# Kernel tuning notes

Measured on AMD Instinct MI355X. Metric: run time of the kernel, lower is better.

The kernel has to match this reference:

```python
import jax, jax.numpy as jnp
import numpy as np

B, T, F, H = 256, 256, 512, 512
DIN = 17  # 16 MLP features + 1 Y_past channel
EPS = 1e-3  # keras LayerNorm/BatchNorm default epsilon


def _glorot(key, shape):
    lim = np.sqrt(6.0 / (shape[0] + shape[-1]))
    return jax.random.uniform(key, shape, jnp.float32, -lim, lim)


def setup_inputs():
    key = jax.random.key(0)
    ks = iter(jax.random.split(key, 48))
    p = {}
    p["x"] = jax.random.normal(next(ks), (B, T, F), jnp.float32)
    p["y_past"] = jax.random.randint(next(ks), (B, T), 0, 11, jnp.int32)
    p["ln_g"] = jnp.ones((F,), jnp.float32); p["ln_b"] = jnp.zeros((F,), jnp.float32)
    for i, (a, b) in enumerate([(F, 128), (128, 64), (64, 32), (32, 16)], 1):
        p[f"w{i}"] = _glorot(next(ks), (a, b)); p[f"b{i}"] = jnp.zeros((b,), jnp.float32)
    for name, d in [("bn1", 128), ("bn2", 16)]:
        p[name + "_g"] = jnp.ones((d,), jnp.float32); p[name + "_b"] = jnp.zeros((d,), jnp.float32)
        p[name + "_m"] = jnp.zeros((d,), jnp.float32); p[name + "_v"] = jnp.ones((d,), jnp.float32)
    for pre, din in [("enc_fwd", DIN), ("enc_bwd", DIN), ("dec", H)]:
        p[pre + "_wx"] = _glorot(next(ks), (din, 4 * H))
        p[pre + "_wh"] = _glorot(next(ks), (H, 4 * H))
        p[pre + "_bias"] = jnp.zeros((4 * H,), jnp.float32)
    for pre in ["proj", "sph", "spc"]:
        p[pre + "_w"] = _glorot(next(ks), (2 * H, H)); p[pre + "_b"] = jnp.zeros((H,), jnp.float32)
    p["out_w"] = _glorot(next(ks), (H, 2)); p["out_b"] = jnp.zeros((2,), jnp.float32)
    return p


def _lstm(x_seq, wx, wh, bias):
    """Keras-order (i,f,g,o) LSTM over [B,T,Din]; returns (hs [B,T,H], hT, cT)."""
    xz = jnp.einsum('btd,dh->bth', x_seq, wx) + bias  # precompute input gates
    h0 = jnp.zeros((x_seq.shape[0], H), x_seq.dtype)
    c0 = jnp.zeros_like(h0)
    def step(carry, xz_t):
        h, c = carry
        z = xz_t + h @ wh
        i, f, g, o = jnp.split(z, 4, axis=-1)
        c = jax.nn.sigmoid(f) * c + jax.nn.sigmoid(i) * jnp.tanh(g)
        h = jax.nn.sigmoid(o) * jnp.tanh(c)
        return (h, c), h
    (hT, cT), hs = jax.lax.scan(step, (h0, c0), jnp.swapaxes(xz, 0, 1))
    return jnp.swapaxes(hs, 0, 1), hT, cT


def _forward(x, ln_g, ln_b, w1, b1, w2, b2, w3, b3, w4, b4,
             bn1_g, bn1_b, bn1_m, bn1_v, bn2_g, bn2_b, bn2_m, bn2_v,
             enc_fwd_wx, enc_fwd_wh, enc_fwd_bias,
             enc_bwd_wx, enc_bwd_wh, enc_bwd_bias,
             dec_wx, dec_wh, dec_bias,
             proj_w, proj_b, sph_w, sph_b, spc_w, spc_b, out_w, out_b, y_past):
    # LayerNorm over feature axis
    mu = jnp.mean(x, -1, keepdims=True)
    var = jnp.var(x, -1, keepdims=True)
    h = (x - mu) * jax.lax.rsqrt(var + EPS) * ln_g + ln_b
    # Dense funnel with inference-mode BatchNorm (dropout is identity)
    h = jax.nn.relu(h @ w1 + b1)
    h = (h - bn1_m) * jax.lax.rsqrt(bn1_v + EPS) * bn1_g + bn1_b
    h = jax.nn.relu(h @ w2 + b2)
    h = jax.nn.relu(h @ w3 + b3)
    h = jax.nn.relu(h @ w4 + b4)
    h = (h - bn2_m) * jax.lax.rsqrt(bn2_v + EPS) * bn2_g + bn2_b
    seq = jnp.concatenate([h, y_past.astype(jnp.float32)[..., None]], axis=-1)  # [B,T,17]
    # Bidirectional LSTM encoder
    hs_f, hf, cf = _lstm(seq, enc_fwd_wx, enc_fwd_wh, enc_fwd_bias)
    hs_b, hb, cb = _lstm(seq[:, ::-1], enc_bwd_wx, enc_bwd_wh, enc_bwd_bias)
    enc = jnp.concatenate([hs_f, hs_b[:, ::-1]], axis=-1)  # [B,T,2H]
    enc = enc @ proj_w + proj_b                             # [B,T,H]
    state_h = jnp.concatenate([hf, hb], -1) @ sph_w + sph_b
    state_c = jnp.concatenate([cf, cb], -1) @ spc_w + spc_b
    # keras Attention (dot-product, unscaled), query = state_h expanded to len 1
    scores = jnp.einsum('bh,bth->bt', state_h, enc)
    attn = jnp.einsum('bt,bth->bh', jax.nn.softmax(scores, axis=-1), enc)  # [B,H]
    # decoder LSTM runs on a length-1 sequence => single cell step
    z = attn @ dec_wx + state_h @ dec_wh + dec_bias
    i, f, g, o = jnp.split(z, 4, axis=-1)
    c = jax.nn.sigmoid(f) * state_c + jax.nn.sigmoid(i) * jnp.tanh(g)
    hdec = jax.nn.sigmoid(o) * jnp.tanh(c)
    return hdec @ out_w + out_b  # [B,2]


def reference(x, y_past, ln_g, ln_b, w1, b1, w2, b2, w3, b3, w4, b4,
              bn1_g, bn1_b, bn1_m, bn1_v, bn2_g, bn2_b, bn2_m, bn2_v,
              enc_fwd_wx, enc_fwd_wh, enc_fwd_bias,
              enc_bwd_wx, enc_bwd_wh, enc_bwd_bias,
              dec_wx, dec_wh, dec_bias,
              proj_w, proj_b, sph_w, sph_b, spc_w, spc_b, out_w, out_b):
    return _forward(x, ln_g, ln_b, w1, b1, w2, b2, w3, b3, w4, b4,
                    bn1_g, bn1_b, bn1_m, bn1_v, bn2_g, bn2_b, bn2_m, bn2_v,
                    enc_fwd_wx, enc_fwd_wh, enc_fwd_bias,
                    enc_bwd_wx, enc_bwd_wh, enc_bwd_bias,
                    dec_wx, dec_wh, dec_bias,
                    proj_w, proj_b, sph_w, sph_b, spc_w, spc_b, out_w, out_b, y_past)
```

## Files before the change

kernel.cpp:

```cpp
#include <hip/hip_runtime.h>
#include <hip/hip_bf16.h>

#define EPSK 1e-3f

using bf16x8 = __attribute__((ext_vector_type(8))) short;
using s16x4  = __attribute__((ext_vector_type(4))) short;
using f32x4  = __attribute__((ext_vector_type(4))) float;
using u32x2  = __attribute__((ext_vector_type(2))) unsigned int;

__device__ __forceinline__ float bf2f(short s) {
    union { unsigned u; float f; } x; x.u = ((unsigned)(unsigned short)s) << 16; return x.f;
}
__device__ __forceinline__ unsigned short f2bfu(float f) {
    union { float f; unsigned u; } x; x.f = f;
    unsigned r = x.u + 0x7fffu + ((x.u >> 16) & 1u);
    return (unsigned short)(r >> 16);
}
__device__ __forceinline__ float sigm(float x) { return 1.0f / (1.0f + __expf(-x)); }
__device__ __forceinline__ float ftanh(float x) {
    float e = __expf(2.0f * x);
    return 1.0f - 2.0f / (e + 1.0f);
}

__device__ __forceinline__ f32x4 load16_coh(const void* p) {
    f32x4 v;
    asm volatile("global_load_dwordx4 %0, %1, off sc0 sc1" : "=v"(v) : "v"(p) : "memory");
    return v;
}
__device__ __forceinline__ void store8_coh(void* p, u32x2 v) {
    asm volatile("global_store_dwordx2 %0, %1, off sc0 sc1" :: "v"(p), "v"(v) : "memory");
}
__device__ __forceinline__ void store8_nt(void* p, u32x2 v) {
    asm volatile("global_store_dwordx2 %0, %1, off nt" :: "v"(p), "v"(v) : "memory");
}


__global__ void cvt_f2b_kernel(__hip_bfloat16* __restrict__ dst, const float* __restrict__ src, int n)
{
    for (int i = blockIdx.x * blockDim.x + threadIdx.x; i < n; i += gridDim.x * blockDim.x)
        dst[i] = __float2bfloat16(src[i]);
}

__global__ void copy_f_kernel(float* __restrict__ dst, const float* __restrict__ src, int n)
{
    for (int i = blockIdx.x * blockDim.x + threadIdx.x; i < n; i += gridDim.x * blockDim.x)
        dst[i] = src[i];
}

#define NTJOBS 11
struct TransJobs {
    const float* src[NTJOBS];
    __hip_bfloat16* dst[NTJOBS];
    int K[NTJOBS], N[NTJOBS], kOff[NTJOBS], KD[NTJOBS];
};

__global__ __launch_bounds__(256)
void trans_tiled_kernel(TransJobs jobs)
{
    const int j = blockIdx.y;
    const int K = jobs.K[j], N = jobs.N[j];
    const int tilesN = (N + 31) >> 5;
    const int tilesK = (K + 31) >> 5;
    if ((int)blockIdx.x >= tilesN * tilesK) return;
    const int tk = blockIdx.x / tilesN, tn = blockIdx.x % tilesN;
    const int kOff = jobs.kOff[j], KD = jobs.KD[j];
    const float* src = jobs.src[j];
    __hip_bfloat16* dst = jobs.dst[j];
    __shared__ float tile[32][33];
    const int tid = threadIdx.x;
    #pragma unroll
    for (int i = 0; i < 4; ++i) {
        int e = i * 256 + tid;
        int r = e >> 5, c = e & 31;
        int k = tk * 32 + r, n = tn * 32 + c;
        tile[r][c] = (k < K && n < N) ? src[(size_t)k * N + n] : 0.f;
    }
    __syncthreads();
    #pragma unroll
    for (int i = 0; i < 4; ++i) {
        int e = i * 256 + tid;
        int rn = e >> 5, ck = e & 31;
        int n = tn * 32 + rn, k = tk * 32 + ck;
        if (k < K && n < N) dst[(size_t)n * KD + kOff + k] = __float2bfloat16(tile[ck][rn]);
    }
}


__global__ __launch_bounds__(256)
void funnel_kernel(const float* __restrict__ x, const int* __restrict__ yp,
                   const float* __restrict__ ln_g, const float* __restrict__ ln_b,
                   const __hip_bfloat16* __restrict__ w1T,
                   const float* __restrict__ b1,
                   const __hip_bfloat16* __restrict__ w2T,
                   const float* __restrict__ b2,
                   const float* __restrict__ w3, const float* __restrict__ b3,
                   const float* __restrict__ w4, const float* __restrict__ b4,
                   const float* __restrict__ bn1g, const float* __restrict__ bn1b,
                   const float* __restrict__ bn1m, const float* __restrict__ bn1v,
                   const float* __restrict__ bn2g, const float* __restrict__ bn2b,
                   const float* __restrict__ bn2m, const float* __restrict__ bn2v,
                   __hip_bfloat16* __restrict__ seqbf)
{
    __shared__ __align__(16) __hip_bfloat16 xn[16][520];
    __shared__ __align__(16) __hip_bfloat16 h1s[16][136];
    __shared__ float h2s[16][64];
    __shared__ float h3s[16][32];
    const int tid = threadIdx.x;
    const int w = tid >> 6, lane = tid & 63;
    const int l15 = lane & 15, l4 = lane >> 4;
    const int g0 = blockIdx.x * 16;

    for (int pp = 0; pp < 4; ++pp) {
        int r = pp * 4 + w;
        const float* xr = x + (size_t)(g0 + r) * 512;
        f32x4 v0 = *(const f32x4*)(xr + lane * 8);
        f32x4 v1 = *(const f32x4*)(xr + lane * 8 + 4);
        float s = v0[0]+v0[1]+v0[2]+v0[3] + v1[0]+v1[1]+v1[2]+v1[3];
        float q = v0[0]*v0[0]+v0[1]*v0[1]+v0[2]*v0[2]+v0[3]*v0[3]
                + v1[0]*v1[0]+v1[1]*v1[1]+v1[2]*v1[2]+v1[3]*v1[3];
        for (int o = 32; o; o >>= 1) { s += __shfl_xor(s, o); q += __shfl_xor(q, o); }
        float mu = s * (1.0f / 512.0f);
        float var = q * (1.0f / 512.0f) - mu * mu;
        float rs = rsqrtf(var + EPSK);
        union { unsigned short s[8]; f32x4 v; } pk;
        #pragma unroll
        for (int j = 0; j < 8; ++j) {
            int c = lane * 8 + j;
            float xv = (j < 4) ? v0[j] : v1[j - 4];
            pk.s[j] = f2bfu((xv - mu) * rs * ln_g[c] + ln_b[c]);
        }
        *(f32x4*)(&xn[r][lane * 8]) = pk.v;
    }
    __syncthreads();

    {
        f32x4 acc[2];
        acc[0] = (f32x4){0.f,0.f,0.f,0.f};
        acc[1] = (f32x4){0.f,0.f,0.f,0.f};
        #pragma unroll
        for (int kc = 0; kc < 16; ++kc) {
            bf16x8 a = *(const bf16x8*)(&xn[l15][kc * 32 + l4 * 8]);
            #pragma unroll
            for (int nf = 0; nf < 2; ++nf) {
                bf16x8 b = *(const bf16x8*)(w1T + (size_t)(w * 32 + nf * 16 + l15) * 512 + kc * 32 + l4 * 8);
                acc[nf] = __builtin_amdgcn_mfma_f32_16x16x32_bf16(a, b, acc[nf], 0, 0, 0);
            }
        }
        #pragma unroll
        for (int nf = 0; nf < 2; ++nf)
            #pragma unroll
            for (int r = 0; r < 4; ++r) {
                int row = l4 * 4 + r;
                int col = w * 32 + nf * 16 + l15;
                float v = fmaxf(acc[nf][r] + b1[col], 0.f);
                v = (v - bn1m[col]) * rsqrtf(bn1v[col] + EPSK) * bn1g[col] + bn1b[col];
                h1s[row][col] = __float2bfloat16(v);
            }
    }
    __syncthreads();

    {
        f32x4 acc = (f32x4){0.f,0.f,0.f,0.f};
        #pragma unroll
        for (int kc = 0; kc < 4; ++kc) {
            bf16x8 a = *(const bf16x8*)(&h1s[l15][kc * 32 + l4 * 8]);
            bf16x8 b = *(const bf16x8*)(w2T + (size_t)(w * 16 + l15) * 128 + kc * 32 + l4 * 8);
            acc = __builtin_amdgcn_mfma_f32_16x16x32_bf16(a, b, acc, 0, 0, 0);
        }
        #pragma unroll
        for (int r = 0; r < 4; ++r) {
            int row = l4 * 4 + r, col = w * 16 + l15;
            h2s[row][col] = fmaxf(acc[r] + b2[col], 0.f);
        }
    }
    __syncthreads();

    const int row = tid >> 4, ci = tid & 15;
    {
        float a0 = b3[ci * 2], a1 = b3[ci * 2 + 1];
        #pragma unroll 4
        for (int k = 0; k < 64; ++k) {
            float xv = h2s[row][k];
            a0 += xv * w3[k * 32 + ci * 2];
            a1 += xv * w3[k * 32 + ci * 2 + 1];
        }
        h3s[row][ci * 2] = fmaxf(a0, 0.f);
        h3s[row][ci * 2 + 1] = fmaxf(a1, 0.f);
    }
    __syncthreads();
    {
        float a = b4[ci];
        #pragma unroll
        for (int k = 0; k < 32; ++k) a += h3s[row][k] * w4[k * 16 + ci];
        float v = fmaxf(a, 0.f);
        v = (v - bn2m[ci]) * rsqrtf(bn2v[ci] + EPSK) * bn2g[ci] + bn2b[ci];
        int g = g0 + row, bb = g >> 8, tt = g & 255;
        __hip_bfloat16* sr = seqbf + ((size_t)tt * 256 + bb) * 32;
        sr[ci] = __float2bfloat16(v);
        sr[16 + ci] = (ci == 0) ? __float2bfloat16((float)yp[g]) : __float2bfloat16(0.f);
    }
}


__global__ void __launch_bounds__(256, 2)
lstm_persistent(const __hip_bfloat16* __restrict__ BTcat,
                const float* __restrict__ biasz,
                const __hip_bfloat16* __restrict__ seqbf,
                __hip_bfloat16* __restrict__ hbuf,
                float* __restrict__ cbuf,
                __hip_bfloat16* __restrict__ Aenc,
                unsigned int* __restrict__ ctrs)
{
    const int bid = blockIdx.x;
    const int g = bid & 15;
    const int dirv = g & 1;
    const int mt = g >> 1;
    const int strip = bid >> 4;
    const int tid = threadIdx.x;
    const int w = tid >> 6;
    const int lane = tid & 63;
    const int l15 = lane & 15, l4 = lane >> 4;

    __shared__ __align__(16) unsigned char Atile[32 * 1152];
    __shared__ __align__(16) float zbuf[2][4][16][36];

    float (*zb)[32][36] = (float (*)[32][36])zbuf;

    bf16x8 bw[2][17];
    {
        const __hip_bfloat16* BT = BTcat + (size_t)dirv * 2048 * 544;
        #pragma unroll
        for (int nf = 0; nf < 2; ++nf) {
            const __hip_bfloat16* bp = BT + (size_t)(w * 512 + strip * 32 + nf * 16 + l15) * 544 + l4 * 8;
            #pragma unroll
            for (int kc = 0; kc < 17; ++kc)
                bw[nf][kc] = *(const bf16x8*)(bp + kc * 32);
        }
    }

    const int rr = tid >> 3;
    const int c0 = (tid & 7) * 4;
    const int hcol0 = strip * 32 + c0;
    const int browE = mt * 32 + rr;
    const float* bias = biasz + dirv * 2048;
    const f32x4 b_i = *(const f32x4*)(bias + hcol0);
    const f32x4 b_f = *(const f32x4*)(bias + 512 + hcol0);
    const f32x4 b_g = *(const f32x4*)(bias + 1024 + hcol0);
    const f32x4 b_o = *(const f32x4*)(bias + 1536 + hcol0);

    float creg[4] = {0.f, 0.f, 0.f, 0.f};
    unsigned int* ctr = ctrs + g * 32;
    const int swzA = l15 & 7;

    for (int t = 0; t < 256; ++t) {
        const int tpos = dirv ? (255 - t) : t;

        {
            const unsigned char* hsrc = (const unsigned char*)
                (hbuf + ((size_t)(t & 1) * 2 + dirv) * 131072 + (size_t)mt * 32 * 512);
            f32x4 hv[8];
            #pragma unroll
            for (int it = 0; it < 8; ++it)
                hv[it] = load16_coh(hsrc + (it * 256 + tid) * 16);
            f32x4 sv;
            if (tid < 128) {
                const __hip_bfloat16* sp = seqbf + ((size_t)tpos * 256 + mt * 32 + (tid >> 2)) * 32 + (tid & 3) * 8;
                sv = *(const f32x4*)sp;
            }
            asm volatile("s_waitcnt vmcnt(0)" ::: "memory");
            #pragma unroll
            for (int it = 0; it < 8; ++it) {
                int c = it * 256 + tid;
                int row = c >> 6, s = c & 63;
                *(f32x4*)(Atile + row * 1152 + ((s ^ (row & 7)) << 4)) = hv[it];
            }
            if (tid < 128) {
                int row = tid >> 2, s = 64 + (tid & 3);
                *(f32x4*)(Atile + row * 1152 + ((s ^ (row & 7)) << 4)) = sv;
            }
        }
        __syncthreads();

        f32x4 acc[2][2];
        acc[0][0] = (f32x4){0.f,0.f,0.f,0.f}; acc[0][1] = (f32x4){0.f,0.f,0.f,0.f};
        acc[1][0] = (f32x4){0.f,0.f,0.f,0.f}; acc[1][1] = (f32x4){0.f,0.f,0.f,0.f};
        #pragma unroll
        for (int kc = 0; kc < 17; ++kc) {
            int swz = ((kc * 4 + l4) ^ swzA) << 4;
            bf16x8 a0 = *(const bf16x8*)(Atile + l15 * 1152 + swz);
            bf16x8 a1 = *(const bf16x8*)(Atile + (16 + l15) * 1152 + swz);
            acc[0][0] = __builtin_amdgcn_mfma_f32_16x16x32_bf16(a0, bw[0][kc], acc[0][0], 0, 0, 0);
            acc[0][1] = __builtin_amdgcn_mfma_f32_16x16x32_bf16(a0, bw[1][kc], acc[0][1], 0, 0, 0);
            acc[1][0] = __builtin_amdgcn_mfma_f32_16x16x32_bf16(a1, bw[0][kc], acc[1][0], 0, 0, 0);
            acc[1][1] = __builtin_amdgcn_mfma_f32_16x16x32_bf16(a1, bw[1][kc], acc[1][1], 0, 0, 0);
        }

        #pragma unroll
        for (int mf = 0; mf < 2; ++mf)
            #pragma unroll
            for (int nf = 0; nf < 2; ++nf)
                #pragma unroll
                for (int r = 0; r < 4; ++r)
                    zb[w][mf * 16 + l4 * 4 + r][nf * 16 + l15] = acc[mf][nf][r];
        __syncthreads();

        {
            f32x4 zi4 = *(const f32x4*)(&zb[0][rr][c0]);
            f32x4 zf4 = *(const f32x4*)(&zb[1][rr][c0]);
            f32x4 zg4 = *(const f32x4*)(&zb[2][rr][c0]);
            f32x4 zo4 = *(const f32x4*)(&zb[3][rr][c0]);
            unsigned short hb[4];
            #pragma unroll
            for (int j = 0; j < 4; ++j) {
                float iv = sigm(zi4[j] + b_i[j]);
                float fv = sigm(zf4[j] + b_f[j]);
                float gv = ftanh(zg4[j] + b_g[j]);
                float ov = sigm(zo4[j] + b_o[j]);
                float cnew = fv * creg[j] + iv * gv;
                creg[j] = cnew;
                hb[j] = f2bfu(ov * ftanh(cnew));
            }
            u32x2 hp;
            hp[0] = (unsigned)hb[0] | ((unsigned)hb[1] << 16);
            hp[1] = (unsigned)hb[2] | ((unsigned)hb[3] << 16);
            __hip_bfloat16* hdst = hbuf + ((size_t)((t + 1) & 1) * 2 + dirv) * 131072;
            store8_coh(hdst + (size_t)browE * 512 + hcol0, hp);
            store8_nt(reinterpret_cast<short*>(Aenc) + ((size_t)browE * 256 + tpos) * 1024 + dirv * 512 + hcol0, hp);
        }

        if (t < 255) {
            asm volatile("s_waitcnt vmcnt(0)" ::: "memory");
            __syncthreads();
            if (tid == 0) {
                __hip_atomic_fetch_add(ctr, 1u, __ATOMIC_RELAXED, __HIP_MEMORY_SCOPE_AGENT);
                unsigned int target = 16u * (unsigned)(t + 1);
                while (__hip_atomic_load(ctr, __ATOMIC_RELAXED, __HIP_MEMORY_SCOPE_AGENT) < target)
                    __builtin_amdgcn_s_sleep(2);
            }
            __syncthreads();
        }
    }

    *(f32x4*)(cbuf + (size_t)dirv * 131072 + (size_t)browE * 512 + hcol0) =
        (f32x4){creg[0], creg[1], creg[2], creg[3]};
}


template<int MT, int KD>
__global__ __launch_bounds__(256)
void dec_cell_kernel(const __hip_bfloat16* __restrict__ Abase,
                     const __hip_bfloat16* __restrict__ BTbase,
                     const float* __restrict__ bias,
                     const float* __restrict__ Cin,
                     float* __restrict__ HdecOut)
{
    constexpr int RB = KD * 2;
    constexpr int MF = MT / 16;
    constexpr int KSTEPS = KD / 32;
    const int strip = blockIdx.x;
    const int mt = blockIdx.y;
    const int tid = threadIdx.x;
    const int w = tid >> 6;
    const int lane = tid & 63;

    __shared__ __align__(16) unsigned char Als[MT * KD * 2];
    __shared__ float zbuf[4][MT][33];

    const __hip_bfloat16* A = Abase + (size_t)(mt * MT) * KD;
    const __hip_bfloat16* BT = BTbase;

    const unsigned char* Ac = (const unsigned char*)A;
    #pragma unroll
    for (int it = 0; it < (MT * KD * 2) / 4096; ++it) {
        int p = it * 4096 + tid * 16;
        int row = p / RB;
        int slot = (p % RB) >> 4;
        int ls = slot ^ (row & 7);
        *(f32x4*)(Als + row * RB + ls * 16) = *(const f32x4*)(Ac + p);
    }
    __syncthreads();

    f32x4 acc[MF][2];
    #pragma unroll
    for (int mf = 0; mf < MF; ++mf)
        #pragma unroll
        for (int nf = 0; nf < 2; ++nf)
            acc[mf][nf] = (f32x4){0.f,0.f,0.f,0.f};

    const int l15 = lane & 15, l4 = lane >> 4;
    #pragma unroll 4
    for (int kc = 0; kc < KSTEPS; ++kc) {
        bf16x8 a[MF], bb[2];
        int kslot = kc * 4 + l4;
        #pragma unroll
        for (int mf = 0; mf < MF; ++mf) {
            int row = mf * 16 + l15;
            a[mf] = *(const bf16x8*)(Als + row * RB + ((kslot ^ (row & 7)) << 4));
        }
        #pragma unroll
        for (int nf = 0; nf < 2; ++nf) {
            int zr = w * 512 + strip * 32 + nf * 16 + l15;
            bb[nf] = *(const bf16x8*)(BT + (size_t)zr * KD + kc * 32 + l4 * 8);
        }
        #pragma unroll
        for (int mf = 0; mf < MF; ++mf)
            #pragma unroll
            for (int nf = 0; nf < 2; ++nf)
                acc[mf][nf] = __builtin_amdgcn_mfma_f32_16x16x32_bf16(a[mf], bb[nf], acc[mf][nf], 0, 0, 0);
    }

    #pragma unroll
    for (int mf = 0; mf < MF; ++mf)
        #pragma unroll
        for (int nf = 0; nf < 2; ++nf)
            #pragma unroll
            for (int r = 0; r < 4; ++r)
                zbuf[w][mf * 16 + l4 * 4 + r][nf * 16 + l15] = acc[mf][nf][r];
    __syncthreads();

    constexpr int NE = MT * 32 / 256;
    #pragma unroll
    for (int e = 0; e < NE; ++e) {
        int idx = e * 256 + tid;
        int r = idx >> 5, col = idx & 31;
        int hcol = strip * 32 + col;
        int brow = mt * MT + r;
        float zi = zbuf[0][r][col] + bias[hcol];
        float zf = zbuf[1][r][col] + bias[512 + hcol];
        float zg = zbuf[2][r][col] + bias[1024 + hcol];
        float zo = zbuf[3][r][col] + bias[1536 + hcol];
        float iv = sigm(zi), fv = sigm(zf), gv = ftanh(zg);
        float cold = Cin[(size_t)brow * 512 + hcol];
        float cnew = fv * cold + iv * gv;
        HdecOut[(size_t)brow * 512 + hcol] = sigm(zo) * ftanh(cnew);
    }
}


__global__ __launch_bounds__(256)
void gemm_kernel(const __hip_bfloat16* __restrict__ A,
                 const __hip_bfloat16* __restrict__ BT,
                 const float* __restrict__ bias,
                 float* __restrict__ outF,
                 int M, int N, int K)
{
    const int tid = threadIdx.x;
    const int wv = tid >> 6, lane = tid & 63;
    const int wr = wv >> 1, wc = wv & 1;
    const int m0 = blockIdx.y * 64, n0 = blockIdx.x * 64;
    const int l15 = lane & 15, l4 = lane >> 4;
    f32x4 acc[2][2];
    #pragma unroll
    for (int i = 0; i < 2; ++i)
        #pragma unroll
        for (int j = 0; j < 2; ++j) acc[i][j] = (f32x4){0.f,0.f,0.f,0.f};
    for (int kc = 0; kc < K / 32; ++kc) {
        bf16x8 a[2], b[2];
        #pragma unroll
        for (int m2 = 0; m2 < 2; ++m2)
            a[m2] = *(const bf16x8*)(A + (size_t)(m0 + wr * 32 + m2 * 16 + l15) * K + kc * 32 + l4 * 8);
        #pragma unroll
        for (int n2 = 0; n2 < 2; ++n2)
            b[n2] = *(const bf16x8*)(BT + (size_t)(n0 + wc * 32 + n2 * 16 + l15) * K + kc * 32 + l4 * 8);
        #pragma unroll
        for (int m2 = 0; m2 < 2; ++m2)
            #pragma unroll
            for (int n2 = 0; n2 < 2; ++n2)
                acc[m2][n2] = __builtin_amdgcn_mfma_f32_16x16x32_bf16(a[m2], b[n2], acc[m2][n2], 0, 0, 0);
    }
    #pragma unroll
    for (int m2 = 0; m2 < 2; ++m2)
        #pragma unroll
        for (int n2 = 0; n2 < 2; ++n2)
            #pragma unroll
            for (int r = 0; r < 4; ++r) {
                int row = m0 + wr * 32 + m2 * 16 + l4 * 4 + r;
                int col = n0 + wc * 32 + n2 * 16 + l15;
                float v = acc[m2][n2][r];
                if (bias) v += bias[col];
                outF[(size_t)row * N + col] = v;
            }
}


__global__ __launch_bounds__(256)
void attn_kernel(const __hip_bfloat16* __restrict__ Aenc,
                 const float* __restrict__ qh,
                 __hip_bfloat16* __restrict__ Aactx)
{
    const int b = blockIdx.x, tid = threadIdx.x;
    __shared__ float qs[1024];
    __shared__ float sc[256];
    __shared__ float wred[4];
    for (int i = tid; i < 1024; i += 256) qs[i] = qh[(size_t)b * 1024 + i];
    __syncthreads();
    const __hip_bfloat16* ar = Aenc + ((size_t)b * 256 + tid) * 1024;
    float s = 0.f;
    for (int j8 = 0; j8 < 128; ++j8) {
        bf16x8 v = *(const bf16x8*)(ar + j8 * 8);
        #pragma unroll
        for (int e = 0; e < 8; ++e) s += bf2f(v[e]) * qs[j8 * 8 + e];
    }
    float m = s;
    for (int o = 32; o; o >>= 1) m = fmaxf(m, __shfl_xor(m, o));
    if ((tid & 63) == 0) wred[tid >> 6] = m;
    __syncthreads();
    m = fmaxf(fmaxf(wred[0], wred[1]), fmaxf(wred[2], wred[3]));
    __syncthreads();
    float ev = __expf(s - m);
    float ss = ev;
    for (int o = 32; o; o >>= 1) ss += __shfl_xor(ss, o);
    if ((tid & 63) == 0) wred[tid >> 6] = ss;
    __syncthreads();
    float tot = wred[0] + wred[1] + wred[2] + wred[3];
    sc[tid] = ev / tot;
    __syncthreads();
    float a0 = 0, a1 = 0, a2 = 0, a3 = 0;
    for (int t2 = 0; t2 < 256; ++t2) {
        float p = sc[t2];
        s16x4 v = *(const s16x4*)(Aenc + ((size_t)b * 256 + t2) * 1024 + tid * 4);
        a0 += p * bf2f(v[0]); a1 += p * bf2f(v[1]); a2 += p * bf2f(v[2]); a3 += p * bf2f(v[3]);
    }
    __hip_bfloat16* dst = Aactx + (size_t)b * 1024 + tid * 4;
    dst[0] = __float2bfloat16(a0); dst[1] = __float2bfloat16(a1);
    dst[2] = __float2bfloat16(a2); dst[3] = __float2bfloat16(a3);
}


__global__ void pack_state_kernel(const __hip_bfloat16* __restrict__ hbuf0,
                                  const float* __restrict__ cbuf,
                                  __hip_bfloat16* __restrict__ Astate,
                                  __hip_bfloat16* __restrict__ Astatec)
{
    int i = blockIdx.x * blockDim.x + threadIdx.x;
    if (i < 262144) {
        int bb = i >> 10, jj = i & 1023;
        int dir = jj >> 9, j = jj & 511;
        size_t src = (size_t)dir * 131072 + bb * 512 + j;
        Astate[i] = hbuf0[src];
        Astatec[i] = __float2bfloat16(cbuf[src]);
    }
}

__global__ void pack_dec_kernel(const float* __restrict__ attnf,
                                const float* __restrict__ sh,
                                __hip_bfloat16* __restrict__ Adec)
{
    int i = blockIdx.x * blockDim.x + threadIdx.x;
    if (i < 262144) {
        int bb = i >> 10, jj = i & 1023;
        float v = (jj < 512) ? attnf[bb * 512 + jj] : sh[bb * 512 + (jj - 512)];
        Adec[i] = __float2bfloat16(v);
    }
}

__global__ void out_kernel(const float* __restrict__ hdec,
                           const float* __restrict__ out_w,
                           const float* __restrict__ out_b,
                           float* __restrict__ out)
{
    int b = blockIdx.x, lane = threadIdx.x;
    float a0 = 0.f, a1 = 0.f;
    for (int h = lane; h < 512; h += 64) {
        float hv = hdec[(size_t)b * 512 + h];
        a0 += hv * out_w[2 * h];
        a1 += hv * out_w[2 * h + 1];
    }
    for (int o = 32; o; o >>= 1) { a0 += __shfl_down(a0, o); a1 += __shfl_down(a1, o); }
    if (lane == 0) { out[2 * b] = a0 + out_b[0]; out[2 * b + 1] = a1 + out_b[1]; }
}


extern "C" void kernel_launch(void* const* d_in, const int* in_sizes, int n_in,
                              void* d_out, int out_size, void* d_ws, size_t ws_size,
                              hipStream_t stream) {
    (void)in_sizes; (void)n_in; (void)out_size; (void)ws_size;
    const float* x        = (const float*)d_in[0];
    const int*   y_past   = (const int*)d_in[1];
    const float* ln_g     = (const float*)d_in[2];
    const float* ln_b     = (const float*)d_in[3];
    const float* w1       = (const float*)d_in[4];
    const float* b1       = (const float*)d_in[5];
    const float* w2       = (const float*)d_in[6];
    const float* b2       = (const float*)d_in[7];
    const float* w3       = (const float*)d_in[8];
    const float* b3       = (const float*)d_in[9];
    const float* w4       = (const float*)d_in[10];
    const float* b4       = (const float*)d_in[11];
    const float* bn1_g    = (const float*)d_in[12];
    const float* bn1_b    = (const float*)d_in[13];
    const float* bn1_m    = (const float*)d_in[14];
    const float* bn1_v    = (const float*)d_in[15];
    const float* bn2_g    = (const float*)d_in[16];
    const float* bn2_b    = (const float*)d_in[17];
    const float* bn2_m    = (const float*)d_in[18];
    const float* bn2_v    = (const float*)d_in[19];
    const float* efwx     = (const float*)d_in[20];
    const float* efwh     = (const float*)d_in[21];
    const float* efbias   = (const float*)d_in[22];
    const float* ebwx     = (const float*)d_in[23];
    const float* ebwh     = (const float*)d_in[24];
    const float* ebbias   = (const float*)d_in[25];
    const float* dec_wx   = (const float*)d_in[26];
    const float* dec_wh   = (const float*)d_in[27];
    const float* dec_bias = (const float*)d_in[28];
    const float* proj_w   = (const float*)d_in[29];
    const float* proj_b   = (const float*)d_in[30];
    const float* sph_w    = (const float*)d_in[31];
    const float* sph_b    = (const float*)d_in[32];
    const float* spc_w    = (const float*)d_in[33];
    const float* spc_b    = (const float*)d_in[34];
    const float* out_w    = (const float*)d_in[35];
    const float* out_b    = (const float*)d_in[36];

    char* wsb = (char*)d_ws;
    size_t off = 0;
    auto alloc = [&](size_t bytes) -> char* {
        char* r = wsb + off;
        off = (off + bytes + 255) & ~(size_t)255;
        return r;
    };
    __hip_bfloat16* BTcat   = (__hip_bfloat16*)alloc(2ull * 2048 * 544 * 2);
    __hip_bfloat16* decT    = (__hip_bfloat16*)alloc(2048ull * 1024 * 2);
    __hip_bfloat16* projT   = (__hip_bfloat16*)alloc(512ull * 1024 * 2);
    __hip_bfloat16* projWb  = (__hip_bfloat16*)alloc(1024ull * 512 * 2);
    __hip_bfloat16* sphT    = (__hip_bfloat16*)alloc(512ull * 1024 * 2);
    __hip_bfloat16* spcT    = (__hip_bfloat16*)alloc(512ull * 1024 * 2);
    __hip_bfloat16* w1T     = (__hip_bfloat16*)alloc(128ull * 512 * 2);
    __hip_bfloat16* w2T     = (__hip_bfloat16*)alloc(64ull * 128 * 2);
    float*          biasz   = (float*)alloc(2ull * 2048 * 4);
    __hip_bfloat16* seqbf   = (__hip_bfloat16*)alloc(256ull * 256 * 32 * 2);
    __hip_bfloat16* hbuf    = (__hip_bfloat16*)alloc(2ull * 2 * 256 * 512 * 2);
    float*          cbuf    = (float*)alloc(2ull * 256 * 512 * 4);
    __hip_bfloat16* Aenc    = (__hip_bfloat16*)alloc(65536ull * 1024 * 2);
    unsigned int*   ctrs    = (unsigned int*)alloc(16ull * 32 * 4);
    __hip_bfloat16* Astate  = (__hip_bfloat16*)alloc(256ull * 1024 * 2);
    __hip_bfloat16* Astatec = (__hip_bfloat16*)alloc(256ull * 1024 * 2);
    float*          state_h = (float*)alloc(256ull * 512 * 4);
    float*          state_c = (float*)alloc(256ull * 512 * 4);
    __hip_bfloat16* Ash     = (__hip_bfloat16*)alloc(256ull * 512 * 2);
    float*          qh      = (float*)alloc(256ull * 1024 * 4);
    __hip_bfloat16* Aactx   = (__hip_bfloat16*)alloc(256ull * 1024 * 2);
    float*          attnf   = (float*)alloc(256ull * 512 * 4);
    __hip_bfloat16* Adec    = (__hip_bfloat16*)alloc(256ull * 1024 * 2);
    float*          hdec    = (float*)alloc(256ull * 512 * 4);

    (void)hipMemsetAsync(BTcat, 0, 2ull * 2048 * 544 * 2, stream);
    {
        TransJobs jobs;
        jobs.src[0]  = efwh;   jobs.dst[0]  = BTcat;              jobs.K[0]  = 512;  jobs.N[0]  = 2048; jobs.kOff[0]  = 0;   jobs.KD[0]  = 544;
        jobs.src[1]  = efwx;   jobs.dst[1]  = BTcat;              jobs.K[1]  = 17;   jobs.N[1]  = 2048; jobs.kOff[1]  = 512; jobs.KD[1]  = 544;
        jobs.src[2]  = ebwh;   jobs.dst[2]  = BTcat + 2048 * 544; jobs.K[2]  = 512;  jobs.N[2]  = 2048; jobs.kOff[2]  = 0;   jobs.KD[2]  = 544;
        jobs.src[3]  = ebwx;   jobs.dst[3]  = BTcat + 2048 * 544; jobs.K[3]  = 17;   jobs.N[3]  = 2048; jobs.kOff[3]  = 512; jobs.KD[3]  = 544;
        jobs.src[4]  = proj_w; jobs.dst[4]  = projT;              jobs.K[4]  = 1024; jobs.N[4]  = 512;  jobs.kOff[4]  = 0;   jobs.KD[4]  = 1024;
        jobs.src[5]  = sph_w;  jobs.dst[5]  = sphT;               jobs.K[5]  = 1024; jobs.N[5]  = 512;  jobs.kOff[5]  = 0;   jobs.KD[5]  = 1024;
        jobs.src[6]  = spc_w;  jobs.dst[6]  = spcT;               jobs.K[6]  = 1024; jobs.N[6]  = 512;  jobs.kOff[6]  = 0;   jobs.KD[6]  = 1024;
        jobs.src[7]  = dec_wx; jobs.dst[7]  = decT;               jobs.K[7]  = 512;  jobs.N[7]  = 2048; jobs.kOff[7]  = 0;   jobs.KD[7]  = 1024;
        jobs.src[8]  = dec_wh; jobs.dst[8]  = decT;               jobs.K[8]  = 512;  jobs.N[8]  = 2048; jobs.kOff[8]  = 512; jobs.KD[8]  = 1024;
        jobs.src[9]  = w1;     jobs.dst[9]  = w1T;                jobs.K[9]  = 512;  jobs.N[9]  = 128;  jobs.kOff[9]  = 0;   jobs.KD[9]  = 512;
        jobs.src[10] = w2;     jobs.dst[10] = w2T;                jobs.K[10] = 128;  jobs.N[10] = 64;   jobs.kOff[10] = 0;   jobs.KD[10] = 128;
        trans_tiled_kernel<<<dim3(1024, NTJOBS), 256, 0, stream>>>(jobs);
    }
    cvt_f2b_kernel<<<1024, 256, 0, stream>>>(projWb, proj_w, 1024 * 512);
    copy_f_kernel<<<8, 256, 0, stream>>>(biasz, efbias, 2048);
    copy_f_kernel<<<8, 256, 0, stream>>>(biasz + 2048, ebbias, 2048);

    (void)hipMemsetAsync(hbuf, 0, 2ull * 256 * 512 * 2, stream);
    (void)hipMemsetAsync(ctrs, 0, 16ull * 32 * 4, stream);

    funnel_kernel<<<4096, 256, 0, stream>>>(x, y_past, ln_g, ln_b,
        w1T, b1, w2T, b2, w3, b3, w4, b4,
        bn1_g, bn1_b, bn1_m, bn1_v, bn2_g, bn2_b, bn2_m, bn2_v, seqbf);

    lstm_persistent<<<dim3(256), dim3(256), 0, stream>>>(
        BTcat, biasz, seqbf, hbuf, cbuf, Aenc, ctrs);

    pack_state_kernel<<<1024, 256, 0, stream>>>(hbuf, cbuf, Astate, Astatec);
    gemm_kernel<<<dim3(8, 4), 256, 0, stream>>>(Astate, sphT, sph_b, state_h, 256, 512, 1024);
    gemm_kernel<<<dim3(8, 4), 256, 0, stream>>>(Astatec, spcT, spc_b, state_c, 256, 512, 1024);
    cvt_f2b_kernel<<<512, 256, 0, stream>>>(Ash, state_h, 256 * 512);

    gemm_kernel<<<dim3(16, 4), 256, 0, stream>>>(Ash, projWb, nullptr, qh, 256, 1024, 512);
    attn_kernel<<<256, 256, 0, stream>>>(Aenc, qh, Aactx);
    gemm_kernel<<<dim3(8, 4), 256, 0, stream>>>(Aactx, projT, proj_b, attnf, 256, 512, 1024);

    pack_dec_kernel<<<1024, 256, 0, stream>>>(attnf, state_h, Adec);
    dec_cell_kernel<32, 1024><<<dim3(16, 8), 256, 0, stream>>>(
        Adec, decT, dec_bias, state_c, hdec);

    out_kernel<<<256, 64, 0, stream>>>(hdec, out_w, out_b, (float*)d_out);
}
```

Baseline: 1.123 ms.

## Split persistent LSTM into 512 blocks of 16 batch rows each

The persistent bidirectional LSTM kernel now launches 512 blocks instead of 256. Each block handles 16 batch rows instead of 32 for its 32-column hidden strip, which gives 32 sync groups of 16 blocks. Per-step work per block halves: one A-fragment row, two MFMA chains, two elements per thread in the gate epilogue, and smaller shared tiles. Two blocks can now share a CU, so one block's sync and load latency can overlap the other's compute. The cost is that every weight strip is loaded into registers by twice as many blocks. All 512 blocks must also be co-resident at two per CU, or the cross-block sync could deadlock.

```diff
diff --git a/kernel.cpp b/kernel.cpp
--- a/kernel.cpp
+++ b/kernel.cpp
@@ -6,6 +6,7 @@
 using bf16x8 = __attribute__((ext_vector_type(8))) short;
 using s16x4  = __attribute__((ext_vector_type(4))) short;
 using f32x4  = __attribute__((ext_vector_type(4))) float;
+using f32x2  = __attribute__((ext_vector_type(2))) float;
 using u32x2  = __attribute__((ext_vector_type(2))) unsigned int;
 
 __device__ __forceinline__ float bf2f(short s) {
@@ -27,11 +28,11 @@
     asm volatile("global_load_dwordx4 %0, %1, off sc0 sc1" : "=v"(v) : "v"(p) : "memory");
     return v;
 }
-__device__ __forceinline__ void store8_coh(void* p, u32x2 v) {
-    asm volatile("global_store_dwordx2 %0, %1, off sc0 sc1" :: "v"(p), "v"(v) : "memory");
-}
-__device__ __forceinline__ void store8_nt(void* p, u32x2 v) {
-    asm volatile("global_store_dwordx2 %0, %1, off nt" :: "v"(p), "v"(v) : "memory");
+__device__ __forceinline__ void store4_coh(void* p, unsigned v) {
+    asm volatile("global_store_dword %0, %1, off sc0 sc1" :: "v"(p), "v"(v) : "memory");
+}
+__device__ __forceinline__ void store4_nt(void* p, unsigned v) {
+    asm volatile("global_store_dword %0, %1, off nt" :: "v"(p), "v"(v) : "memory");
 }
 
 
@@ -212,19 +213,17 @@
                 unsigned int* __restrict__ ctrs)
 {
     const int bid = blockIdx.x;
-    const int g = bid & 15;
+    const int g = bid >> 4;
     const int dirv = g & 1;
-    const int mt = g >> 1;
-    const int strip = bid >> 4;
+    const int mt16 = g >> 1;
+    const int strip = bid & 15;
     const int tid = threadIdx.x;
     const int w = tid >> 6;
     const int lane = tid & 63;
     const int l15 = lane & 15, l4 = lane >> 4;
 
-    __shared__ __align__(16) unsigned char Atile[32 * 1152];
-    __shared__ __align__(16) float zbuf[2][4][16][36];
-
-    float (*zb)[32][36] = (float (*)[32][36])zbuf;
+    __shared__ __align__(16) unsigned char Atile[16 * 1152];
+    __shared__ __align__(16) float zbuf[4][16][36];
 
     bf16x8 bw[2][17];
     {
@@ -238,17 +237,17 @@
         }
     }
 
-    const int rr = tid >> 3;
-    const int c0 = (tid & 7) * 4;
+    const int rr = tid >> 4;
+    const int c0 = (tid & 15) * 2;
     const int hcol0 = strip * 32 + c0;
-    const int browE = mt * 32 + rr;
+    const int browE = mt16 * 16 + rr;
     const float* bias = biasz + dirv * 2048;
-    const f32x4 b_i = *(const f32x4*)(bias + hcol0);
-    const f32x4 b_f = *(const f32x4*)(bias + 512 + hcol0);
-    const f32x4 b_g = *(const f32x4*)(bias + 1024 + hcol0);
-    const f32x4 b_o = *(const f32x4*)(bias + 1536 + hcol0);
-
-    float creg[4] = {0.f, 0.f, 0.f, 0.f};
+    const float bi0 = bias[hcol0],        bi1 = bias[hcol0 + 1];
+    const float bf0 = bias[512 + hcol0],  bf1 = bias[512 + hcol0 + 1];
+    const float bg0 = bias[1024 + hcol0], bg1 = bias[1024 + hcol0 + 1];
+    const float bo0 = bias[1536 + hcol0], bo1 = bias[1536 + hcol0 + 1];
+
+    float creg0 = 0.f, creg1 = 0.f;
     unsigned int* ctr = ctrs + g * 32;
     const int swzA = l15 & 7;
 
@@ -257,75 +256,62 @@
 
         {
             const unsigned char* hsrc = (const unsigned char*)
-                (hbuf + ((size_t)(t & 1) * 2 + dirv) * 131072 + (size_t)mt * 32 * 512);
-            f32x4 hv[8];
-            #pragma unroll
-            for (int it = 0; it < 8; ++it)
+                (hbuf + ((size_t)(t & 1) * 2 + dirv) * 131072 + (size_t)mt16 * 16 * 512);
+            f32x4 hv[4];
+            #pragma unroll
+            for (int it = 0; it < 4; ++it)
                 hv[it] = load16_coh(hsrc + (it * 256 + tid) * 16);
             f32x4 sv;
-            if (tid < 128) {
-                const __hip_bfloat16* sp = seqbf + ((size_t)tpos * 256 + mt * 32 + (tid >> 2)) * 32 + (tid & 3) * 8;
+            if (tid < 64) {
+                const __hip_bfloat16* sp = seqbf + ((size_t)tpos * 256 + mt16 * 16 + (tid >> 2)) * 32 + (tid & 3) * 8;
                 sv = *(const f32x4*)sp;
             }
             asm volatile("s_waitcnt vmcnt(0)" ::: "memory");
             #pragma unroll
-            for (int it = 0; it < 8; ++it) {
+            for (int it = 0; it < 4; ++it) {
                 int c = it * 256 + tid;
                 int row = c >> 6, s = c & 63;
                 *(f32x4*)(Atile + row * 1152 + ((s ^ (row & 7)) << 4)) = hv[it];
             }
-            if (tid < 128) {
+            if (tid < 64) {
                 int row = tid >> 2, s = 64 + (tid & 3);
                 *(f32x4*)(Atile + row * 1152 + ((s ^ (row & 7)) << 4)) = sv;
             }
         }
         __syncthreads();
 
-        f32x4 acc[2][2];
-        acc[0][0] = (f32x4){0.f,0.f,0.f,0.f}; acc[0][1] = (f32x4){0.f,0.f,0.f,0.f};
-        acc[1][0] = (f32x4){0.f,0.f,0.f,0.f}; acc[1][1] = (f32x4){0.f,0.f,0.f,0.f};
+        f32x4 acc0 = (f32x4){0.f,0.f,0.f,0.f};
+        f32x4 acc1 = (f32x4){0.f,0.f,0.f,0.f};
         #pragma unroll
         for (int kc = 0; kc < 17; ++kc) {
             int swz = ((kc * 4 + l4) ^ swzA) << 4;
-            bf16x8 a0 = *(const bf16x8*)(Atile + l15 * 1152 + swz);
-            bf16x8 a1 = *(const bf16x8*)(Atile + (16 + l15) * 1152 + swz);
-            acc[0][0] = __builtin_amdgcn_mfma_f32_16x16x32_bf16(a0, bw[0][kc], acc[0][0], 0, 0, 0);
-            acc[0][1] = __builtin_amdgcn_mfma_f32_16x16x32_bf16(a0, bw[1][kc], acc[0][1], 0, 0, 0);
-            acc[1][0] = __builtin_amdgcn_mfma_f32_16x16x32_bf16(a1, bw[0][kc], acc[1][0], 0, 0, 0);
-            acc[1][1] = __builtin_amdgcn_mfma_f32_16x16x32_bf16(a1, bw[1][kc], acc[1][1], 0, 0, 0);
-        }
-
-        #pragma unroll
-        for (int mf = 0; mf < 2; ++mf)
-            #pragma unroll
-            for (int nf = 0; nf < 2; ++nf)
-                #pragma unroll
-                for (int r = 0; r < 4; ++r)
-                    zb[w][mf * 16 + l4 * 4 + r][nf * 16 + l15] = acc[mf][nf][r];
+            bf16x8 a = *(const bf16x8*)(Atile + l15 * 1152 + swz);
+            acc0 = __builtin_amdgcn_mfma_f32_16x16x32_bf16(a, bw[0][kc], acc0, 0, 0, 0);
+            acc1 = __builtin_amdgcn_mfma_f32_16x16x32_bf16(a, bw[1][kc], acc1, 0, 0, 0);
+        }
+
+        #pragma unroll
+        for (int r = 0; r < 4; ++r) {
+            zbuf[w][l4 * 4 + r][l15]      = acc0[r];
+            zbuf[w][l4 * 4 + r][16 + l15] = acc1[r];
+        }
         __syncthreads();
 
+        unsigned hp;
         {
-            f32x4 zi4 = *(const f32x4*)(&zb[0][rr][c0]);
-            f32x4 zf4 = *(const f32x4*)(&zb[1][rr][c0]);
-            f32x4 zg4 = *(const f32x4*)(&zb[2][rr][c0]);
-            f32x4 zo4 = *(const f32x4*)(&zb[3][rr][c0]);
-            unsigned short hb[4];
-            #pragma unroll
-            for (int j = 0; j < 4; ++j) {
-                float iv = sigm(zi4[j] + b_i[j]);
-                float fv = sigm(zf4[j] + b_f[j]);
-                float gv = ftanh(zg4[j] + b_g[j]);
-                float ov = sigm(zo4[j] + b_o[j]);
-                float cnew = fv * creg[j] + iv * gv;
-                creg[j] = cnew;
-                hb[j] = f2bfu(ov * ftanh(cnew));
-            }
-            u32x2 hp;
-            hp[0] = (unsigned)hb[0] | ((unsigned)hb[1] << 16);
-            hp[1] = (unsigned)hb[2] | ((unsigned)hb[3] << 16);
+            f32x2 zi2 = *(const f32x2*)(&zbuf[0][rr][c0]);
+            f32x2 zf2 = *(const f32x2*)(&zbuf[1][rr][c0]);
+            f32x2 zg2 = *(const f32x2*)(&zbuf[2][rr][c0]);
+            f32x2 zo2 = *(const f32x2*)(&zbuf[3][rr][c0]);
+            float c0n = sigm(zf2[0] + bf0) * creg0 + sigm(zi2[0] + bi0) * ftanh(zg2[0] + bg0);
+            float c1n = sigm(zf2[1] + bf1) * creg1 + sigm(zi2[1] + bi1) * ftanh(zg2[1] + bg1);
+            creg0 = c0n; creg1 = c1n;
+            float h0 = sigm(zo2[0] + bo0) * ftanh(c0n);
+            float h1 = sigm(zo2[1] + bo1) * ftanh(c1n);
+            hp = (unsigned)f2bfu(h0) | ((unsigned)f2bfu(h1) << 16);
             __hip_bfloat16* hdst = hbuf + ((size_t)((t + 1) & 1) * 2 + dirv) * 131072;
-            store8_coh(hdst + (size_t)browE * 512 + hcol0, hp);
-            store8_nt(reinterpret_cast<short*>(Aenc) + ((size_t)browE * 256 + tpos) * 1024 + dirv * 512 + hcol0, hp);
+            store4_coh(hdst + (size_t)browE * 512 + hcol0, hp);
+            store4_nt(reinterpret_cast<short*>(Aenc) + ((size_t)browE * 256 + tpos) * 1024 + dirv * 512 + hcol0, hp);
         }
 
         if (t < 255) {
@@ -341,8 +327,10 @@
         }
     }
 
-    *(f32x4*)(cbuf + (size_t)dirv * 131072 + (size_t)browE * 512 + hcol0) =
-        (f32x4){creg[0], creg[1], creg[2], creg[3]};
+    {
+        float* cd = cbuf + (size_t)dirv * 131072 + (size_t)browE * 512 + hcol0;
+        cd[0] = creg0; cd[1] = creg1;
+    }
 }
 
 
@@ -633,7 +621,7 @@
     __hip_bfloat16* hbuf    = (__hip_bfloat16*)alloc(2ull * 2 * 256 * 512 * 2);
     float*          cbuf    = (float*)alloc(2ull * 256 * 512 * 4);
     __hip_bfloat16* Aenc    = (__hip_bfloat16*)alloc(65536ull * 1024 * 2);
-    unsigned int*   ctrs    = (unsigned int*)alloc(16ull * 32 * 4);
+    unsigned int*   ctrs    = (unsigned int*)alloc(32ull * 32 * 4);
     __hip_bfloat16* Astate  = (__hip_bfloat16*)alloc(256ull * 1024 * 2);
     __hip_bfloat16* Astatec = (__hip_bfloat16*)alloc(256ull * 1024 * 2);
     float*          state_h = (float*)alloc(256ull * 512 * 4);
@@ -666,13 +654,13 @@
     copy_f_kernel<<<8, 256, 0, stream>>>(biasz + 2048, ebbias, 2048);
 
     (void)hipMemsetAsync(hbuf, 0, 2ull * 256 * 512 * 2, stream);
-    (void)hipMemsetAsync(ctrs, 0, 16ull * 32 * 4, stream);
+    (void)hipMemsetAsync(ctrs, 0, 32ull * 32 * 4, stream);
 
     funnel_kernel<<<4096, 256, 0, stream>>>(x, y_past, ln_g, ln_b,
         w1T, b1, w2T, b2, w3, b3, w4, b4,
         bn1_g, bn1_b, bn1_m, bn1_v, bn2_g, bn2_b, bn2_m, bn2_v, seqbf);
 
-    lstm_persistent<<<dim3(256), dim3(256), 0, stream>>>(
+    lstm_persistent<<<dim3(512), dim3(256), 0, stream>>>(
         BTcat, biasz, seqbf, hbuf, cbuf, Aenc, ctrs);
 
     pack_state_kernel<<<1024, 256, 0, stream>>>(hbuf, cbuf, Astate, Astatec);
```

Measured after the change: 1.089 ms. 3.0% less time.
